# Performance work log

Measured on AMD Instinct MI355X. Metric: run time of the kernel, lower is better.

Reference implementation:

```python
import jax, jax.numpy as jnp
import numpy as np

N_GRAPHS = 256
EPS = 1e-5


def _bn(x, g, b):
    # training-mode BatchNorm1d: biased batch statistics
    m = jnp.mean(x, axis=0)
    v = jnp.mean((x - m) ** 2, axis=0)
    return (x - m) * jax.lax.rsqrt(v + EPS) * g + b


def _gcn_conv(x, W, b, src, dst, dinv, n_nodes):
    # GCNConv: D^{-1/2} (A + I) D^{-1/2} X W + b
    h = x @ W  # [N, H]
    coef = dinv[src] * dinv[dst]  # [E]
    msg = h[src] * coef[:, None]  # [E, H]
    agg = jax.ops.segment_sum(msg, dst, num_segments=n_nodes)
    agg = agg + h * (dinv * dinv)[:, None]  # self-loop term
    return agg + b


def setup_inputs() -> dict:
    key = jax.random.key(0)
    ks = jax.random.split(key, 20)
    N, E, D, H, C = 50000, 600000, 128, 128, 10
    L = 3  # num_conv_layers
    x = jax.random.normal(ks[0], (N, D), dtype=jnp.float32)
    edge_index = jax.random.randint(ks[1], (2, E), 0, N, dtype=jnp.int64)
    batch = jnp.sort(jax.random.randint(ks[2], (N,), 0, N_GRAPHS, dtype=jnp.int64))

    def xavier(k, shape):
        fan_in, fan_out = shape[0], shape[1]
        lim = float(np.sqrt(6.0 / (fan_in + fan_out)))
        return jax.random.uniform(k, shape, jnp.float32, -lim, lim)

    return {
        "x": x,
        "edge_index": edge_index,
        "batch": batch,
        "bn_feat_g": jnp.ones((D,), jnp.float32),
        "bn_feat_b": jnp.full((D,), 1e-4, jnp.float32),
        "conv_feat_W": xavier(ks[3], (D, H)),
        "conv_feat_b": jnp.zeros((H,), jnp.float32),
        "conv_W": jnp.stack([xavier(ks[4 + i], (H, H)) for i in range(L)]),
        "conv_b": jnp.zeros((L, H), jnp.float32),
        "bn_conv_g": jnp.ones((L, H), jnp.float32),
        "bn_conv_b": jnp.full((L, H), 1e-4, jnp.float32),
        "gate_W1": xavier(ks[8], (H, H)),
        "gate_b1": jnp.zeros((H,), jnp.float32),
        "gate_W2": xavier(ks[9], (H, 1)),
        "gate_b2": jnp.zeros((1,), jnp.float32),
        "fc_W": xavier(ks[10], (H, H)),
        "fc_b": jnp.zeros((H,), jnp.float32),
        "bn_fc_g": jnp.ones((H,), jnp.float32),
        "bn_fc_b": jnp.full((H,), 1e-4, jnp.float32),
        "cls_W": xavier(ks[11], (H, C)),
        "cls_b": jnp.zeros((C,), jnp.float32),
    }


def reference(x, edge_index, batch, bn_feat_g, bn_feat_b, conv_feat_W, conv_feat_b,
              conv_W, conv_b, bn_conv_g, bn_conv_b, gate_W1, gate_b1, gate_W2,
              gate_b2, fc_W, fc_b, bn_fc_g, bn_fc_b, cls_W, cls_b):
    N = x.shape[0]
    src, dst = edge_index[0], edge_index[1]
    # degree incl. self-loop (edge weights = 1)
    deg = jax.ops.segment_sum(jnp.ones_like(src, dtype=x.dtype), dst, num_segments=N) + 1.0
    dinv = jax.lax.rsqrt(deg)

    h = _bn(x, bn_feat_g, bn_feat_b)
    h = jax.nn.relu(_gcn_conv(h, conv_feat_W, conv_feat_b, src, dst, dinv, N))
    for i in range(conv_W.shape[0]):
        h = jax.nn.relu(_gcn_conv(_bn(h, bn_conv_g[i], bn_conv_b[i]),
                                  conv_W[i], conv_b[i], src, dst, dinv, N))
    gate = jax.nn.sigmoid(jax.nn.relu(h @ gate_W1 + gate_b1) @ gate_W2 + gate_b2)  # [N,1]
    g = jax.ops.segment_sum(h * gate, batch, num_segments=N_GRAPHS)  # [G, H]
    g = jax.nn.relu(_bn(g, bn_fc_g, bn_fc_b) @ fc_W + fc_b)
    logits = g @ cls_W + cls_b
    return jax.nn.log_softmax(logits, axis=-1)
```

## Files before the change

### kernel.cpp

```cpp
#include <hip/hip_runtime.h>
#include <hip/hip_fp16.h>

typedef unsigned short u16;
typedef unsigned int u32;
typedef __attribute__((ext_vector_type(8))) short short8;
typedef __attribute__((ext_vector_type(4))) float floatx4;

#define EPSI 1e-5f

__device__ __forceinline__ float b2f(u16 h) { return __uint_as_float(((u32)h) << 16); }
__device__ __forceinline__ u16 f2b(float f) {
    u32 u = __float_as_uint(f);
    return (u16)((u + 0x7fffu + ((u >> 16) & 1u)) >> 16);
}
__device__ __forceinline__ u32 pack2(float a, float b) {
    return (u32)f2b(a) | ((u32)f2b(b) << 16);
}
__device__ __forceinline__ float ldf(const void* p, int i, int fm) {
    if (fm == 1) return b2f(((const u16*)p)[i]);
    if (fm == 2) return __half2float(__ushort_as_half(((const u16*)p)[i]));
    return ((const float*)p)[i];
}
__device__ __forceinline__ int ldi(const void* p, int i, int im) {
    return im ? ((const int*)p)[2 * i] : ((const int*)p)[i];
}

template <typename T>
__device__ __forceinline__ void ntst(T* p, T v) {
    __builtin_nontemporal_store(v, p);
}

__device__ __forceinline__ void acc8(float* a, int4 v, float w) {
    u32 x = (u32)v.x, y = (u32)v.y, z = (u32)v.z, q = (u32)v.w;
    a[0] += b2f((u16)x) * w;
    a[1] += b2f((u16)(x >> 16)) * w;
    a[2] += b2f((u16)y) * w;
    a[3] += b2f((u16)(y >> 16)) * w;
    a[4] += b2f((u16)z) * w;
    a[5] += b2f((u16)(z >> 16)) * w;
    a[6] += b2f((u16)q) * w;
    a[7] += b2f((u16)(q >> 16)) * w;
}

__global__ void init_kernel(u32* zp, int nz, const void* ones, const void* ei, int* flags) {
    int i = blockIdx.x * 256 + threadIdx.x;
    if (i < nz) zp[i] = 0;
    if (blockIdx.x == 0 && threadIdx.x == 0) {
        u32 w = ((const u32*)ones)[0];
        int fm = 0;
        if (w == 0x3F803F80u) fm = 1;
        else if (w == 0x3C003C00u) fm = 2;
        const u32* e = (const u32*)ei;
        int all0 = 1;
        for (int k = 0; k < 16; ++k)
            if (e[2 * k + 1] != 0u) all0 = 0;
        flags[0] = fm;
        flags[1] = all0;
    }
}

__global__ void bigprep_kernel(const void* __restrict__ ei, int* __restrict__ cnt, int E,
                               const void* __restrict__ batch, int* __restrict__ bounds, int N,
                               int EB, const void* __restrict__ x, u32* __restrict__ A2,
                               float* __restrict__ stats0, const void* __restrict__ gW1,
                               const void* __restrict__ gb1, u16* __restrict__ Wtg,
                               float* __restrict__ bias2g, const void* __restrict__ cfW,
                               const void* __restrict__ cW, u16* __restrict__ Wt4,
                               const void* __restrict__ fcW, float* __restrict__ fcWf,
                               const void* __restrict__ clsW, float* __restrict__ clsWf,
                               const void* __restrict__ fcb, float* __restrict__ fcbf,
                               const void* __restrict__ clsb, float* __restrict__ clsbf,
                               const void* __restrict__ gW2, float* __restrict__ gW2f,
                               const void* __restrict__ gb2, float* __restrict__ gb2f,
                               const void* __restrict__ cfb, const void* __restrict__ cvb,
                               float* __restrict__ biasf, u16* __restrict__ rank,
                               const int* __restrict__ flags) {
    int fm = flags[0];
    int bid = blockIdx.x, t = threadIdx.x;
    if (bid < EB) {
        int im = flags[1];
        int g = bid * 256 + t;
        if (g < E) {
            int r = atomicAdd(&cnt[ldi(ei, E + g, im)], 1);
            rank[g] = (u16)r;
        }
        if (g < N) {
            int b = ldi(batch, g, im);
            if (g == 0) {
                for (int q = 0; q <= b; ++q) bounds[q] = 0;
            } else {
                int bp = ldi(batch, g - 1, im);
                for (int q = bp + 1; q <= b; ++q) bounds[q] = g;
            }
            if (g == N - 1) {
                for (int q = b + 1; q <= 256; ++q) bounds[q] = N;
            }
        }
        return;
    }
    int pid = bid - EB;
    if (pid < 1024) {
        int np = N * 64;
        float s0 = 0.f, s1 = 0.f, q0 = 0.f, q1 = 0.f;
        if (fm == 1) {
            const u32* xs = (const u32*)x;
            for (int j = pid * 256 + t; j < np; j += 1024 * 256) {
                u32 w = xs[j];
                ntst(&A2[j], w);
                float v0 = b2f((u16)w), v1 = b2f((u16)(w >> 16));
                s0 += v0;
                q0 += v0 * v0;
                s1 += v1;
                q1 += v1 * v1;
            }
        } else if (fm == 0) {
            const float2* xs2 = (const float2*)x;
            for (int j = pid * 256 + t; j < np; j += 1024 * 256) {
                float2 v = xs2[j];
                ntst(&A2[j], pack2(v.x, v.y));
                s0 += v.x;
                q0 += v.x * v.x;
                s1 += v.y;
                q1 += v.y * v.y;
            }
        } else {
            for (int j = pid * 256 + t; j < np; j += 1024 * 256) {
                float v0 = ldf(x, 2 * j, fm);
                float v1 = ldf(x, 2 * j + 1, fm);
                ntst(&A2[j], pack2(v0, v1));
                s0 += v0;
                q0 += v0 * v0;
                s1 += v1;
                q1 += v1 * v1;
            }
        }
        __shared__ float2 sh[256];
        sh[t] = make_float2(s0, s1);
        __syncthreads();
        float* so = stats0 + (pid & 15) * 256;
        if (t < 64) {
            float a = 0.f, b = 0.f;
#pragma unroll
            for (int w = 0; w < 4; ++w) {
                float2 v = sh[t + w * 64];
                a += v.x;
                b += v.y;
            }
            atomicAdd(&so[2 * t], a);
            atomicAdd(&so[2 * t + 1], b);
        }
        __syncthreads();
        sh[t] = make_float2(q0, q1);
        __syncthreads();
        if (t < 64) {
            float a = 0.f, b = 0.f;
#pragma unroll
            for (int w = 0; w < 4; ++w) {
                float2 v = sh[t + w * 64];
                a += v.x;
                b += v.y;
            }
            atomicAdd(&so[128 + 2 * t], a);
            atomicAdd(&so[128 + 2 * t + 1], b);
        }
    } else if (pid < 1152) {
        int n = pid - 1024;
        if (t < 128) Wtg[n * 128 + t] = f2b(ldf(gW1, t * 128 + n, fm));
        if (t == 0) bias2g[n] = ldf(gb1, n, fm);
    } else if (pid < 1216) {
        int task = pid - 1152;
        int mat = task >> 4, tile = task & 15;
        int tr = (tile >> 2) * 32, tc = (tile & 3) * 32;
        const void* src = mat == 0 ? cfW : cW;
        int soff = mat == 0 ? 0 : (mat - 1) * 16384;
        __shared__ float tb[32][33];
#pragma unroll
        for (int i = 0; i < 4; ++i) {
            int o = t * 4 + i;
            int r = o >> 5, c = o & 31;
            tb[r][c] = ldf(src, soff + (tr + r) * 128 + tc + c, fm);
        }
        __syncthreads();
        u16* dst = Wt4 + mat * 16384;
#pragma unroll
        for (int i = 0; i < 4; ++i) {
            int o = t * 4 + i;
            int nr = o >> 5, kc = o & 31;
            dst[(tc + nr) * 128 + tr + kc] = f2b(tb[kc][nr]);
        }
    } else if (pid < 1224) {
        int base = (pid - 1216) * 2048;
        for (int i = t; i < 2048; i += 256) fcWf[base + i] = ldf(fcW, base + i, fm);
    } else {
        for (int i = t; i < 1280; i += 256) clsWf[i] = ldf(clsW, i, fm);
        for (int i = t; i < 512; i += 256)
            biasf[i] = (i < 128) ? ldf(cfb, i, fm) : ldf(cvb, i - 128, fm);
        if (t < 128) {
            fcbf[t] = ldf(fcb, t, fm);
            gW2f[t] = ldf(gW2, t, fm);
        }
        if (t < 10) clsbf[t] = ldf(clsb, t, fm);
        if (t == 0) gb2f[0] = ldf(gb2, 0, fm);
    }
}

__global__ void scan_kernel(const int* __restrict__ cnt, int* __restrict__ row_start, int n) {
    int b = blockIdx.x, t = threadIdx.x;
    __shared__ int sh[256];
    const int4* c4 = (const int4*)cnt;
    int lim4 = b * 256;
    int acc = 0;
    for (int i = t; i < lim4; i += 256) {
        int4 v = c4[i];
        acc += v.x + v.y + v.z + v.w;
    }
    sh[t] = acc;
    __syncthreads();
    for (int o = 128; o > 0; o >>= 1) {
        if (t < o) sh[t] += sh[t + o];
        __syncthreads();
    }
    int pre = sh[0];
    __syncthreads();
    int base = b * 1024 + t * 4;
    int v[4];
    int s = 0;
#pragma unroll
    for (int j = 0; j < 4; ++j) {
        int idx = base + j;
        v[j] = (idx < n) ? cnt[idx] : 0;
        s += v[j];
    }
    sh[t] = s;
    __syncthreads();
    for (int o = 1; o < 256; o <<= 1) {
        int add = (t >= o) ? sh[t - o] : 0;
        __syncthreads();
        sh[t] += add;
        __syncthreads();
    }
    int run = pre + sh[t] - s;
#pragma unroll
    for (int j = 0; j < 4; ++j) {
        int idx = base + j;
        run += v[j];
        if (idx < n) row_start[idx + 1] = run;
    }
    if (b == 0 && t == 0) row_start[0] = 0;
}

__global__ __launch_bounds__(256) void mfma_fill_kernel(
    const u16* __restrict__ A, const u16* __restrict__ Wt, const float* __restrict__ stats,
    const void* __restrict__ bng, const void* __restrict__ bnb, u16* __restrict__ C, int N,
    int mmgrid, const void* __restrict__ ei, const int* __restrict__ row_start,
    const u16* __restrict__ rank, const int* __restrict__ cnt, u32* __restrict__ edges, int E,
    const int* __restrict__ flags) {
    int t = threadIdx.x;
    if ((int)blockIdx.x >= mmgrid) {
        int im = flags[1];
        int e = (blockIdx.x - mmgrid) * 256 + t;
        if (e < E) {
            int s = ldi(ei, e, im);
            int d = ldi(ei, E + e, im);
            int p = row_start[d] + (int)rank[e];
            float ds = rsqrtf((float)cnt[s] + 1.0f);
            edges[p] = (u32)s | ((u32)__half_as_ushort(__float2half_rn(ds)) << 16);
        }
        return;
    }
    int fm = flags[0];
    __shared__ float scs[128], shs[128];
    if (t < 128) {
        float ms = 0.f, qs = 0.f;
#pragma unroll
        for (int c = 0; c < 16; ++c) {
            ms += stats[c * 256 + t];
            qs += stats[c * 256 + 128 + t];
        }
        float m = ms / (float)N;
        float var = qs / (float)N - m * m;
        float rs = rsqrtf(var + EPSI);
        float sc = rs * ldf(bng, t, fm);
        scs[t] = sc;
        shs[t] = ldf(bnb, t, fm) - m * sc;
    }
    __syncthreads();
    int wid = t >> 6, lane = t & 63;
    int m16 = lane & 15, q = lane >> 4;
    int row0 = blockIdx.x * 64 + wid * 16;
    if (row0 >= N) return;
    int arow = row0 + m16;
    floatx4 acc[8];
#pragma unroll
    for (int i = 0; i < 8; ++i) acc[i] = (floatx4){0.f, 0.f, 0.f, 0.f};
#pragma unroll
    for (int kc = 0; kc < 4; ++kc) {
        short8 af;
        if (arow < N) {
            short8 raw = *(const short8*)&A[(size_t)arow * 128 + kc * 32 + q * 8];
            int k0 = kc * 32 + q * 8;
#pragma unroll
            for (int j = 0; j < 8; ++j)
                af[j] = (short)f2b(b2f((u16)raw[j]) * scs[k0 + j] + shs[k0 + j]);
        } else {
#pragma unroll
            for (int j = 0; j < 8; ++j) af[j] = 0;
        }
#pragma unroll
        for (int nt = 0; nt < 8; ++nt) {
            short8 bf = *(const short8*)&Wt[(nt * 16 + m16) * 128 + kc * 32 + q * 8];
            acc[nt] = __builtin_amdgcn_mfma_f32_16x16x32_bf16(af, bf, acc[nt], 0, 0, 0);
        }
    }
#pragma unroll
    for (int nt = 0; nt < 8; ++nt) {
#pragma unroll
        for (int reg = 0; reg < 4; ++reg) {
            int r = row0 + q * 4 + reg;
            if (r < N) C[(size_t)r * 128 + nt * 16 + m16] = f2b(acc[nt][reg]);
        }
    }
}

__global__ __launch_bounds__(256) void mfma_mm_kernel(
    const u16* __restrict__ A, const u16* __restrict__ Wt, const float* __restrict__ stats,
    const void* __restrict__ bng, const void* __restrict__ bnb, int poff,
    const float* __restrict__ bias2, u16* __restrict__ C, float* __restrict__ gate,
    const float* __restrict__ gW2f, const float* __restrict__ gb2f, int N, int mode,
    const int* __restrict__ flags) {
    int t = threadIdx.x;
    __shared__ float scs[128], shs[128];
    if (stats && t < 128) {
        int fm = flags[0];
        float ms = 0.f, qs = 0.f;
#pragma unroll
        for (int c = 0; c < 16; ++c) {
            ms += stats[c * 256 + t];
            qs += stats[c * 256 + 128 + t];
        }
        float m = ms / (float)N;
        float var = qs / (float)N - m * m;
        float rs = rsqrtf(var + EPSI);
        float sc = rs * ldf(bng, poff + t, fm);
        scs[t] = sc;
        shs[t] = ldf(bnb, poff + t, fm) - m * sc;
    }
    __syncthreads();
    int wid = t >> 6, lane = t & 63;
    int m16 = lane & 15, q = lane >> 4;
    int row0 = blockIdx.x * 64 + wid * 16;
    if (row0 >= N) return;
    int arow = row0 + m16;
    floatx4 acc[8];
#pragma unroll
    for (int i = 0; i < 8; ++i) acc[i] = (floatx4){0.f, 0.f, 0.f, 0.f};
#pragma unroll
    for (int kc = 0; kc < 4; ++kc) {
        short8 af;
        if (arow < N) {
            if (stats) {
                short8 raw = *(const short8*)&A[(size_t)arow * 128 + kc * 32 + q * 8];
                int k0 = kc * 32 + q * 8;
#pragma unroll
                for (int j = 0; j < 8; ++j)
                    af[j] = (short)f2b(b2f((u16)raw[j]) * scs[k0 + j] + shs[k0 + j]);
            } else {
                af = *(const short8*)&A[(size_t)arow * 128 + kc * 32 + q * 8];
            }
        } else {
#pragma unroll
            for (int j = 0; j < 8; ++j) af[j] = 0;
        }
#pragma unroll
        for (int nt = 0; nt < 8; ++nt) {
            short8 bf = *(const short8*)&Wt[(nt * 16 + m16) * 128 + kc * 32 + q * 8];
            acc[nt] = __builtin_amdgcn_mfma_f32_16x16x32_bf16(af, bf, acc[nt], 0, 0, 0);
        }
    }
    if (mode == 0) {
#pragma unroll
        for (int nt = 0; nt < 8; ++nt) {
#pragma unroll
            for (int reg = 0; reg < 4; ++reg) {
                int r = row0 + q * 4 + reg;
                if (r < N) C[(size_t)r * 128 + nt * 16 + m16] = f2b(acc[nt][reg]);
            }
        }
    } else {
        float p[4] = {0.f, 0.f, 0.f, 0.f};
#pragma unroll
        for (int nt = 0; nt < 8; ++nt) {
            float b2v = bias2[nt * 16 + m16];
            float w2v = gW2f[nt * 16 + m16];
#pragma unroll
            for (int reg = 0; reg < 4; ++reg)
                p[reg] += fmaxf(acc[nt][reg] + b2v, 0.0f) * w2v;
        }
        float gb = gb2f[0];
#pragma unroll
        for (int reg = 0; reg < 4; ++reg) {
            float v = p[reg];
            v += __shfl_xor(v, 1);
            v += __shfl_xor(v, 2);
            v += __shfl_xor(v, 4);
            v += __shfl_xor(v, 8);
            if (m16 == 0) {
                int r = row0 + q * 4 + reg;
                if (r < N) gate[r] = 1.0f / (1.0f + expf(-(v + gb)));
            }
        }
    }
}

__global__ __launch_bounds__(512) void agg_kernel(
    const u32* __restrict__ C2, const int* __restrict__ row_start,
    const u32* __restrict__ edges, const float* __restrict__ biasf, int boff,
    u32* __restrict__ A2, float* __restrict__ statsOut, int N) {
    int t = threadIdx.x;
    int wid = t >> 6, lane = t & 63;
    int g = lane >> 4, p = lane & 15;
    int n = blockIdx.x * 8 + wid;
    __shared__ float xch[8][128];
    __shared__ float2 sh[512];
    float acc[8];
#pragma unroll
    for (int j = 0; j < 8; ++j) acc[j] = 0.f;
    float dinv_d = 1.f;
    if (n < N) {
        int rs = row_start[n], re = row_start[n + 1];
        dinv_d = rsqrtf((float)(re - rs) + 1.0f);
        if (g == 0) {
            int4 s = *(const int4*)&C2[(size_t)n * 64 + p * 4];
            acc8(acc, s, dinv_d);
        }
        for (int e = rs; e < re; e += 16) {
            int iA = e + g, iB = e + 4 + g, iC = e + 8 + g, iD = e + 12 + g;
            u32 eA = edges[iA < re ? iA : re - 1];
            u32 eB = edges[iB < re ? iB : re - 1];
            u32 eC = edges[iC < re ? iC : re - 1];
            u32 eD = edges[iD < re ? iD : re - 1];
            int4 vA = *(const int4*)&C2[(size_t)(eA & 0xFFFFu) * 64 + p * 4];
            int4 vB = *(const int4*)&C2[(size_t)(eB & 0xFFFFu) * 64 + p * 4];
            int4 vC = *(const int4*)&C2[(size_t)(eC & 0xFFFFu) * 64 + p * 4];
            int4 vD = *(const int4*)&C2[(size_t)(eD & 0xFFFFu) * 64 + p * 4];
            float wA = iA < re ? __half2float(__ushort_as_half((u16)(eA >> 16))) : 0.f;
            float wB = iB < re ? __half2float(__ushort_as_half((u16)(eB >> 16))) : 0.f;
            float wC = iC < re ? __half2float(__ushort_as_half((u16)(eC >> 16))) : 0.f;
            float wD = iD < re ? __half2float(__ushort_as_half((u16)(eD >> 16))) : 0.f;
            acc8(acc, vA, wA);
            acc8(acc, vB, wB);
            acc8(acc, vC, wC);
            acc8(acc, vD, wD);
        }
    }
#pragma unroll
    for (int j = 0; j < 8; ++j) {
        acc[j] += __shfl_xor(acc[j], 16);
        acc[j] += __shfl_xor(acc[j], 32);
    }
    if (g == 0) {
#pragma unroll
        for (int j = 0; j < 8; ++j) xch[wid][p * 8 + j] = acc[j];
    }
    __syncthreads();
    float ax = 0.f, ay = 0.f;
    if (n < N) {
        float2 bv = ((const float2*)(biasf + boff))[lane];
        float2 v = ((const float2*)xch[wid])[lane];
        ax = fmaxf(v.x * dinv_d + bv.x, 0.0f);
        ay = fmaxf(v.y * dinv_d + bv.y, 0.0f);
        ntst(&A2[(size_t)n * 64 + lane], pack2(ax, ay));
    }
    if (!statsOut) return;
    sh[t] = make_float2(ax, ay);
    __syncthreads();
    float* so = statsOut + (blockIdx.x & 15) * 256;
    if (t < 64) {
        float a = 0.f, b = 0.f;
#pragma unroll
        for (int w = 0; w < 8; ++w) {
            float2 v = sh[t + w * 64];
            a += v.x;
            b += v.y;
        }
        atomicAdd(&so[2 * t], a);
        atomicAdd(&so[2 * t + 1], b);
    }
    __syncthreads();
    sh[t] = make_float2(ax * ax, ay * ay);
    __syncthreads();
    if (t < 64) {
        float a = 0.f, b = 0.f;
#pragma unroll
        for (int w = 0; w < 8; ++w) {
            float2 v = sh[t + w * 64];
            a += v.x;
            b += v.y;
        }
        atomicAdd(&so[128 + 2 * t], a);
        atomicAdd(&so[128 + 2 * t + 1], b);
    }
}

__global__ void pool_kernel(const u32* __restrict__ A2, const float* __restrict__ gate,
                            const int* __restrict__ bounds, float* __restrict__ pooled,
                            float* __restrict__ statsP) {
    int g = blockIdx.x;
    int t = threadIdx.x;
    int f2 = t & 63, grp = t >> 6;
    int s = bounds[g], e = bounds[g + 1];
    __shared__ float2 sh[256];
    float ax = 0.f, ay = 0.f;
    int r = s + grp;
    for (; r + 4 < e; r += 8) {
        u32 v0 = A2[(size_t)r * 64 + f2];
        u32 v1 = A2[(size_t)(r + 4) * 64 + f2];
        float g0 = gate[r], g1 = gate[r + 4];
        ax += b2f((u16)v0) * g0;
        ay += b2f((u16)(v0 >> 16)) * g0;
        ax += b2f((u16)v1) * g1;
        ay += b2f((u16)(v1 >> 16)) * g1;
    }
    if (r < e) {
        u32 v0 = A2[(size_t)r * 64 + f2];
        float g0 = gate[r];
        ax += b2f((u16)v0) * g0;
        ay += b2f((u16)(v0 >> 16)) * g0;
    }
    sh[t] = make_float2(ax, ay);
    __syncthreads();
    if (t < 64) {
        float2 a = sh[t], b = sh[t + 64], c = sh[t + 128], d = sh[t + 192];
        float x = a.x + b.x + c.x + d.x;
        float y = a.y + b.y + c.y + d.y;
        ((float2*)(pooled + g * 128))[t] = make_float2(x, y);
        float* so = statsP + (g & 7) * 256;
        atomicAdd(&so[2 * t], x);
        atomicAdd(&so[2 * t + 1], y);
        atomicAdd(&so[128 + 2 * t], x * x);
        atomicAdd(&so[128 + 2 * t + 1], y * y);
    }
}

__global__ __launch_bounds__(256) void fc_cls_kernel(
    const float* __restrict__ pooled, const float* __restrict__ statsP,
    const void* __restrict__ bng, const void* __restrict__ bnb,
    const float* __restrict__ fcWf, const float* __restrict__ fcbf,
    const float* __restrict__ clsWf, const float* __restrict__ clsbf, void* __restrict__ out,
    const int* __restrict__ flags) {
    int fm = flags[0];
    int g = blockIdx.x, t = threadIdx.x;
    __shared__ float pv[128];
    __shared__ float red[256];
    __shared__ float fco[128];
    __shared__ float lg[10];
    __shared__ float redv[2];
    if (t < 128) {
        float ms = 0.f, qs = 0.f;
#pragma unroll
        for (int c = 0; c < 8; ++c) {
            ms += statsP[c * 256 + t];
            qs += statsP[c * 256 + 128 + t];
        }
        float m = ms / 256.0f;
        float var = qs / 256.0f - m * m;
        float rs = rsqrtf(var + EPSI);
        float sc = rs * ldf(bng, t, fm);
        pv[t] = pooled[g * 128 + t] * sc + (ldf(bnb, t, fm) - m * sc);
    }
    __syncthreads();
    {
        int j = t & 127, half = t >> 7;
        float acc = 0.f;
        int k0 = half * 64;
#pragma unroll 8
        for (int k = k0; k < k0 + 64; ++k) acc += pv[k] * fcWf[k * 128 + j];
        red[t] = acc;
    }
    __syncthreads();
    if (t < 128) fco[t] = fmaxf(red[t] + red[t + 128] + fcbf[t], 0.0f);
    __syncthreads();
    if (t < 10) {
        float a = clsbf[t];
#pragma unroll 8
        for (int k = 0; k < 128; ++k) a += fco[k] * clsWf[k * 10 + t];
        lg[t] = a;
    }
    __syncthreads();
    if (t == 0) {
        float mx = lg[0];
        for (int j = 1; j < 10; ++j) mx = fmaxf(mx, lg[j]);
        float se = 0.f;
        for (int j = 0; j < 10; ++j) se += expf(lg[j] - mx);
        redv[0] = mx;
        redv[1] = logf(se);
    }
    __syncthreads();
    if (t < 10) {
        float v = lg[t] - redv[0] - redv[1];
        if (fm == 1) ((u16*)out)[g * 10 + t] = f2b(v);
        else if (fm == 2) ((u16*)out)[g * 10 + t] = __half_as_ushort(__float2half(v));
        else ((float*)out)[g * 10 + t] = v;
    }
}

extern "C" void kernel_launch(void* const* d_in, const int* in_sizes, int n_in,
                              void* d_out, int out_size, void* d_ws, size_t ws_size,
                              hipStream_t stream) {
    const void* x = d_in[0];
    const void* ei = d_in[1];
    const void* batch = d_in[2];
    const void* bn_feat_g = d_in[3];
    const void* bn_feat_b = d_in[4];
    const void* conv_feat_W = d_in[5];
    const void* conv_feat_b = d_in[6];
    const void* conv_W = d_in[7];
    const void* conv_b = d_in[8];
    const void* bn_conv_g = d_in[9];
    const void* bn_conv_b = d_in[10];
    const void* gate_W1 = d_in[11];
    const void* gate_b1 = d_in[12];
    const void* gate_W2 = d_in[13];
    const void* gate_b2 = d_in[14];
    const void* fc_W = d_in[15];
    const void* fc_b = d_in[16];
    const void* bn_fc_g = d_in[17];
    const void* bn_fc_b = d_in[18];
    const void* cls_W = d_in[19];
    const void* cls_b = d_in[20];

    const int N = in_sizes[2];
    const int E = in_sizes[1] / 2;
    const int NB = (N + 1023) / 1024;
    const int EB = ((E > N ? E : N) + 255) / 256;

    u32* ws = (u32*)d_ws;
    size_t off = 0;
    auto alloc = [&](size_t n) {
        size_t o = off;
        off += (n + 63) & ~(size_t)63;
        return o;
    };
    size_t o_cnt = alloc(N);
    size_t o_stats = alloc(5 * 4096);
    size_t o_statsP = alloc(2048);
    size_t zero_end = off;
    size_t o_flags = alloc(16);
    size_t o_rs = alloc((size_t)N + 1);
    size_t o_edges = alloc((size_t)E);
    size_t o_rank = alloc(((size_t)E + 1) / 2);
    size_t o_wtg = alloc(128 * 128 / 2);
    size_t o_b2g = alloc(128);
    size_t o_Wt4 = alloc(4 * 16384 / 2);
    size_t o_fcW = alloc(16384);
    size_t o_fcb = alloc(128);
    size_t o_clsW = alloc(1280);
    size_t o_clsb = alloc(16);
    size_t o_gW2 = alloc(128);
    size_t o_gb2 = alloc(16);
    size_t o_biasf = alloc(512);
    size_t o_gate = alloc(N);
    size_t o_bnd = alloc(257);
    size_t o_pool = alloc(256 * 128);
    size_t o_A = alloc((size_t)N * 64);
    size_t o_C = alloc((size_t)N * 64);
    (void)ws_size;
    (void)n_in;
    (void)out_size;

    int* cnt = (int*)(ws + o_cnt);
    float* stats = (float*)(ws + o_stats);
    float* statsP = (float*)(ws + o_statsP);
    int* flags = (int*)(ws + o_flags);
    int* row_start = (int*)(ws + o_rs);
    u32* edges = (u32*)(ws + o_edges);
    u16* rank = (u16*)(ws + o_rank);
    u16* Wtg = (u16*)(ws + o_wtg);
    float* bias2g = (float*)(ws + o_b2g);
    u16* Wt4 = (u16*)(ws + o_Wt4);
    float* fcWf = (float*)(ws + o_fcW);
    float* fcbf = (float*)(ws + o_fcb);
    float* clsWf = (float*)(ws + o_clsW);
    float* clsbf = (float*)(ws + o_clsb);
    float* gW2f = (float*)(ws + o_gW2);
    float* gb2f = (float*)(ws + o_gb2);
    float* biasf = (float*)(ws + o_biasf);
    float* gateb = (float*)(ws + o_gate);
    int* bnd = (int*)(ws + o_bnd);
    float* pooled = (float*)(ws + o_pool);
    u16* A = (u16*)(ws + o_A);
    u16* C = (u16*)(ws + o_C);

    int nz = (int)zero_end;
    init_kernel<<<(nz + 255) / 256, 256, 0, stream>>>(ws, nz, bn_feat_g, ei, flags);
    bigprep_kernel<<<EB + 1225, 256, 0, stream>>>(
        ei, cnt, E, batch, bnd, N, EB, x, (u32*)A, stats, gate_W1, gate_b1, Wtg, bias2g,
        conv_feat_W, conv_W, Wt4, fc_W, fcWf, cls_W, clsWf, fc_b, fcbf, cls_b, clsbf, gate_W2,
        gW2f, gate_b2, gb2f, conv_feat_b, conv_b, biasf, rank, flags);
    scan_kernel<<<NB, 256, 0, stream>>>(cnt, row_start, N);

    int mmgrid = (N + 63) / 64;
    int agggrid = (N + 7) / 8;
    mfma_fill_kernel<<<mmgrid + EB, 256, 0, stream>>>(A, Wt4, stats, bn_feat_g, bn_feat_b, C, N,
                                                      mmgrid, ei, row_start, rank, cnt, edges,
                                                      E, flags);
    for (int l = 0; l < 4; ++l) {
        if (l > 0)
            mfma_mm_kernel<<<mmgrid, 256, 0, stream>>>(
                A, Wt4 + (size_t)l * 16384, stats + (size_t)l * 4096, bn_conv_g, bn_conv_b,
                (l - 1) * 128, nullptr, C, nullptr, nullptr, nullptr, N, 0, flags);
        float* so = (l < 3) ? stats + (size_t)(l + 1) * 4096 : nullptr;
        agg_kernel<<<agggrid, 512, 0, stream>>>((const u32*)C, row_start, edges, biasf, l * 128,
                                                (u32*)A, so, N);
    }

    mfma_mm_kernel<<<mmgrid, 256, 0, stream>>>(A, Wtg, nullptr, nullptr, nullptr, 0, bias2g,
                                               nullptr, gateb, gW2f, gb2f, N, 2, flags);
    pool_kernel<<<256, 256, 0, stream>>>((const u32*)A, gateb, bnd, pooled, statsP);
    fc_cls_kernel<<<256, 256, 0, stream>>>(pooled, statsP, bn_fc_g, bn_fc_b, fcWf, fcbf, clsWf,
                                           clsbf, d_out, flags);
}
```

Before: 443.7 us.

## Make aggregation kernel grid-stride and spread BN-stat atomics over more copies

The aggregation kernel now runs a capped grid of 2560 blocks. Each block loops over several 8-node groups and accumulates BatchNorm sums and squares in registers before one reduction and atomic flush per block. Previously every one of about 6250 blocks issued its own atomics. The partial-stat buffer copies also grow from 16 to 64 to reduce atomic contention. In exchange, consumers must now sum 64 copies of the stats instead of 16, and the loop adds a second barrier per iteration.

Measured after the change: 440.0 us (median of 2 runs). No clear change (-0.8%).

```diff
diff --git a/kernel.cpp b/kernel.cpp
--- a/kernel.cpp
+++ b/kernel.cpp
@@ -7,6 +7,7 @@
 typedef __attribute__((ext_vector_type(4))) float floatx4;
 
 #define EPSI 1e-5f
+#define NCOPY 64
 
 __device__ __forceinline__ float b2f(u16 h) { return __uint_as_float(((u32)h) << 16); }
 __device__ __forceinline__ u16 f2b(float f) {
@@ -137,7 +138,7 @@
         __shared__ float2 sh[256];
         sh[t] = make_float2(s0, s1);
         __syncthreads();
-        float* so = stats0 + (pid & 15) * 256;
+        float* so = stats0 + (pid & (NCOPY - 1)) * 256;
         if (t < 64) {
             float a = 0.f, b = 0.f;
 #pragma unroll
@@ -273,7 +274,7 @@
     if (t < 128) {
         float ms = 0.f, qs = 0.f;
 #pragma unroll
-        for (int c = 0; c < 16; ++c) {
+        for (int c = 0; c < NCOPY; ++c) {
             ms += stats[c * 256 + t];
             qs += stats[c * 256 + 128 + t];
         }
@@ -334,7 +335,7 @@
         int fm = flags[0];
         float ms = 0.f, qs = 0.f;
 #pragma unroll
-        for (int c = 0; c < 16; ++c) {
+        for (int c = 0; c < NCOPY; ++c) {
             ms += stats[c * 256 + t];
             qs += stats[c * 256 + 128 + t];
         }
@@ -419,62 +420,71 @@
     int t = threadIdx.x;
     int wid = t >> 6, lane = t & 63;
     int g = lane >> 4, p = lane & 15;
-    int n = blockIdx.x * 8 + wid;
     __shared__ float xch[8][128];
     __shared__ float2 sh[512];
-    float acc[8];
-#pragma unroll
-    for (int j = 0; j < 8; ++j) acc[j] = 0.f;
-    float dinv_d = 1.f;
-    if (n < N) {
-        int rs = row_start[n], re = row_start[n + 1];
-        dinv_d = rsqrtf((float)(re - rs) + 1.0f);
+    float s0 = 0.f, s1 = 0.f, q0 = 0.f, q1 = 0.f;
+    int ngrp = (N + 7) / 8;
+    for (int gi = blockIdx.x; gi < ngrp; gi += gridDim.x) {
+        int n = gi * 8 + wid;
+        float acc[8];
+#pragma unroll
+        for (int j = 0; j < 8; ++j) acc[j] = 0.f;
+        float dinv_d = 1.f;
+        if (n < N) {
+            int rs = row_start[n], re = row_start[n + 1];
+            dinv_d = rsqrtf((float)(re - rs) + 1.0f);
+            if (g == 0) {
+                int4 s = *(const int4*)&C2[(size_t)n * 64 + p * 4];
+                acc8(acc, s, dinv_d);
+            }
+            for (int e = rs; e < re; e += 16) {
+                int iA = e + g, iB = e + 4 + g, iC = e + 8 + g, iD = e + 12 + g;
+                u32 eA = edges[iA < re ? iA : re - 1];
+                u32 eB = edges[iB < re ? iB : re - 1];
+                u32 eC = edges[iC < re ? iC : re - 1];
+                u32 eD = edges[iD < re ? iD : re - 1];
+                int4 vA = *(const int4*)&C2[(size_t)(eA & 0xFFFFu) * 64 + p * 4];
+                int4 vB = *(const int4*)&C2[(size_t)(eB & 0xFFFFu) * 64 + p * 4];
+                int4 vC = *(const int4*)&C2[(size_t)(eC & 0xFFFFu) * 64 + p * 4];
+                int4 vD = *(const int4*)&C2[(size_t)(eD & 0xFFFFu) * 64 + p * 4];
+                float wA = iA < re ? __half2float(__ushort_as_half((u16)(eA >> 16))) : 0.f;
+                float wB = iB < re ? __half2float(__ushort_as_half((u16)(eB >> 16))) : 0.f;
+                float wC = iC < re ? __half2float(__ushort_as_half((u16)(eC >> 16))) : 0.f;
+                float wD = iD < re ? __half2float(__ushort_as_half((u16)(eD >> 16))) : 0.f;
+                acc8(acc, vA, wA);
+                acc8(acc, vB, wB);
+                acc8(acc, vC, wC);
+                acc8(acc, vD, wD);
+            }
+        }
+#pragma unroll
+        for (int j = 0; j < 8; ++j) {
+            acc[j] += __shfl_xor(acc[j], 16);
+            acc[j] += __shfl_xor(acc[j], 32);
+        }
         if (g == 0) {
-            int4 s = *(const int4*)&C2[(size_t)n * 64 + p * 4];
-            acc8(acc, s, dinv_d);
-        }
-        for (int e = rs; e < re; e += 16) {
-            int iA = e + g, iB = e + 4 + g, iC = e + 8 + g, iD = e + 12 + g;
-            u32 eA = edges[iA < re ? iA : re - 1];
-            u32 eB = edges[iB < re ? iB : re - 1];
-            u32 eC = edges[iC < re ? iC : re - 1];
-            u32 eD = edges[iD < re ? iD : re - 1];
-            int4 vA = *(const int4*)&C2[(size_t)(eA & 0xFFFFu) * 64 + p * 4];
-            int4 vB = *(const int4*)&C2[(size_t)(eB & 0xFFFFu) * 64 + p * 4];
-            int4 vC = *(const int4*)&C2[(size_t)(eC & 0xFFFFu) * 64 + p * 4];
-            int4 vD = *(const int4*)&C2[(size_t)(eD & 0xFFFFu) * 64 + p * 4];
-            float wA = iA < re ? __half2float(__ushort_as_half((u16)(eA >> 16))) : 0.f;
-            float wB = iB < re ? __half2float(__ushort_as_half((u16)(eB >> 16))) : 0.f;
-            float wC = iC < re ? __half2float(__ushort_as_half((u16)(eC >> 16))) : 0.f;
-            float wD = iD < re ? __half2float(__ushort_as_half((u16)(eD >> 16))) : 0.f;
-            acc8(acc, vA, wA);
-            acc8(acc, vB, wB);
-            acc8(acc, vC, wC);
-            acc8(acc, vD, wD);
-        }
-    }
-#pragma unroll
-    for (int j = 0; j < 8; ++j) {
-        acc[j] += __shfl_xor(acc[j], 16);
-        acc[j] += __shfl_xor(acc[j], 32);
-    }
-    if (g == 0) {
-#pragma unroll
-        for (int j = 0; j < 8; ++j) xch[wid][p * 8 + j] = acc[j];
-    }
-    __syncthreads();
-    float ax = 0.f, ay = 0.f;
-    if (n < N) {
-        float2 bv = ((const float2*)(biasf + boff))[lane];
-        float2 v = ((const float2*)xch[wid])[lane];
-        ax = fmaxf(v.x * dinv_d + bv.x, 0.0f);
-        ay = fmaxf(v.y * dinv_d + bv.y, 0.0f);
-        ntst(&A2[(size_t)n * 64 + lane], pack2(ax, ay));
+#pragma unroll
+            for (int j = 0; j < 8; ++j) xch[wid][p * 8 + j] = acc[j];
+        }
+        __syncthreads();
+        float ax = 0.f, ay = 0.f;
+        if (n < N) {
+            float2 bv = ((const float2*)(biasf + boff))[lane];
+            float2 v = ((const float2*)xch[wid])[lane];
+            ax = fmaxf(v.x * dinv_d + bv.x, 0.0f);
+            ay = fmaxf(v.y * dinv_d + bv.y, 0.0f);
+            ntst(&A2[(size_t)n * 64 + lane], pack2(ax, ay));
+        }
+        s0 += ax;
+        s1 += ay;
+        q0 += ax * ax;
+        q1 += ay * ay;
+        __syncthreads();
     }
     if (!statsOut) return;
-    sh[t] = make_float2(ax, ay);
-    __syncthreads();
-    float* so = statsOut + (blockIdx.x & 15) * 256;
+    sh[t] = make_float2(s0, s1);
+    __syncthreads();
+    float* so = statsOut + (blockIdx.x & (NCOPY - 1)) * 256;
     if (t < 64) {
         float a = 0.f, b = 0.f;
 #pragma unroll
@@ -487,7 +497,7 @@
         atomicAdd(&so[2 * t + 1], b);
     }
     __syncthreads();
-    sh[t] = make_float2(ax * ax, ay * ay);
+    sh[t] = make_float2(q0, q1);
     __syncthreads();
     if (t < 64) {
         float a = 0.f, b = 0.f;
@@ -642,7 +652,7 @@
         return o;
     };
     size_t o_cnt = alloc(N);
-    size_t o_stats = alloc(5 * 4096);
+    size_t o_stats = alloc(5 * NCOPY * 256);
     size_t o_statsP = alloc(2048);
     size_t zero_end = off;
     size_t o_flags = alloc(16);
@@ -700,16 +710,17 @@
     scan_kernel<<<NB, 256, 0, stream>>>(cnt, row_start, N);
 
     int mmgrid = (N + 63) / 64;
-    int agggrid = (N + 7) / 8;
+    int ngrp = (N + 7) / 8;
+    int agggrid = ngrp < 2560 ? ngrp : 2560;
     mfma_fill_kernel<<<mmgrid + EB, 256, 0, stream>>>(A, Wt4, stats, bn_feat_g, bn_feat_b, C, N,
                                                       mmgrid, ei, row_start, rank, cnt, edges,
                                                       E, flags);
     for (int l = 0; l < 4; ++l) {
         if (l > 0)
             mfma_mm_kernel<<<mmgrid, 256, 0, stream>>>(
-                A, Wt4 + (size_t)l * 16384, stats + (size_t)l * 4096, bn_conv_g, bn_conv_b,
-                (l - 1) * 128, nullptr, C, nullptr, nullptr, nullptr, N, 0, flags);
-        float* so = (l < 3) ? stats + (size_t)(l + 1) * 4096 : nullptr;
+                A, Wt4 + (size_t)l * 16384, stats + (size_t)l * (NCOPY * 256), bn_conv_g,
+                bn_conv_b, (l - 1) * 128, nullptr, C, nullptr, nullptr, nullptr, N, 0, flags);
+        float* so = (l < 3) ? stats + (size_t)(l + 1) * (NCOPY * 256) : nullptr;
         agg_kernel<<<agggrid, 512, 0, stream>>>((const u32*)C, row_start, edges, biasf, l * 128,
                                                 (u32*)A, so, N);
     }
```
